# Optimization experiments

Measured on AMD Instinct MI355X. Metric: run time of the kernel, lower is better.

## Reference

```python
import jax, jax.numpy as jnp
import numpy as np

HEAD_SIZE = 8
QK_DIM = 512
V_DIM = 512
N = 4096
ATT_DIM = QK_DIM // HEAD_SIZE  # 64
SCALE = ATT_DIM ** (-0.5)
NEG_FILL = jnp.float32(-9e15)


def setup_inputs() -> dict:
    key = jax.random.key(0)
    k1, k2, k3, k4 = jax.random.split(key, 4)
    x1 = jax.random.normal(k1, (N, QK_DIM), dtype=jnp.float32)
    x2 = jax.random.normal(k2, (N, QK_DIM), dtype=jnp.float32)
    v = jax.random.normal(k3, (N, V_DIM), dtype=jnp.float32)
    adj = jax.random.randint(k4, (N, N), 0, 2, dtype=jnp.int32)
    return {"x1": x1, "x2": x2, "v": v, "adj": adj}


def reference(x1, x2, v, adj):
    n = x1.shape[0]
    # [N, H, d] -> [H, N, d]
    q = x1.reshape(n, HEAD_SIZE, -1).transpose(1, 0, 2) * SCALE
    k = x2.reshape(n, HEAD_SIZE, -1).transpose(1, 0, 2)
    vv = v.reshape(n, HEAD_SIZE, -1).transpose(1, 0, 2)
    # [H, N, N] dense scores, masked by adjacency (broadcast over heads)
    scores = jnp.einsum('hnd,hmd->hnm', q, k)
    scores = jnp.where(adj > 0, scores, NEG_FILL)
    attn = jax.nn.softmax(scores, axis=-1)
    out = jnp.einsum('hnm,hmd->hnd', attn, vv)
    # [H, N, d] -> [N, H*d]
    return out.transpose(1, 0, 2).reshape(n, -1)
```

## Files before the change

kernel.cpp:

```cpp
#include <hip/hip_runtime.h>

#define NN 4096
#define HEADS 8
#define DD 64
#define QKD 512

typedef __attribute__((ext_vector_type(8))) short short8;
typedef __attribute__((ext_vector_type(4))) float f32x4;
typedef __attribute__((ext_vector_type(4))) float float4v;
typedef __attribute__((ext_vector_type(4))) int int4v;
typedef unsigned int u32;
typedef unsigned short u16;
typedef unsigned long long u64;

union U8 { u16 u[8]; short8 s; };
union U4 { u32 u[4]; short8 s; };

__device__ __forceinline__ u16 f2bf(float f) {
  u32 u = __float_as_uint(f);
  u += 0x7fffu + ((u >> 16) & 1u);
  return (u16)(u >> 16);
}

__device__ __forceinline__ u32 cvtpk(float lo, float hi) {
  u32 d;
  asm("v_cvt_pk_bf16_f32 %0, %1, %2" : "=v"(d) : "v"(lo), "v"(hi));
  return d;
}

#define GLL(src, dst) __builtin_amdgcn_global_load_lds( \
    (const __attribute__((address_space(1))) void*)(src), \
    (__attribute__((address_space(3))) void*)(dst), 16, 0, 0)

__global__ __launch_bounds__(256) void prepass_fused(
    const float* __restrict__ x2, const float* __restrict__ v,
    const int* __restrict__ adj,
    u16* __restrict__ Kbt, u16* __restrict__ Vbt, u64* __restrict__ At)
{
  __shared__ u16 Vtmp[64][80];
  const int b = blockIdx.x;
  const int t = threadIdx.x;

  if (b < 4096) {
    const int row = b;
    const int* src = adj + (size_t)row * NN;
    int4v a0 = *(const int4v*)(src + t * 16);
    int4v a1 = *(const int4v*)(src + t * 16 + 4);
    int4v a2 = *(const int4v*)(src + t * 16 + 8);
    int4v a3 = *(const int4v*)(src + t * 16 + 12);
    u32 bits =
        (u32)(a0.x > 0)         | ((u32)(a0.y > 0) << 1)  |
        ((u32)(a0.z > 0) << 2)  | ((u32)(a0.w > 0) << 3)  |
        ((u32)(a1.x > 0) << 4)  | ((u32)(a1.y > 0) << 5)  |
        ((u32)(a1.z > 0) << 6)  | ((u32)(a1.w > 0) << 7)  |
        ((u32)(a2.x > 0) << 8)  | ((u32)(a2.y > 0) << 9)  |
        ((u32)(a2.z > 0) << 10) | ((u32)(a2.w > 0) << 11) |
        ((u32)(a3.x > 0) << 12) | ((u32)(a3.y > 0) << 13) |
        ((u32)(a3.z > 0) << 14) | ((u32)(a3.w > 0) << 15);
    unsigned char* AB = (unsigned char*)Vtmp;
    *(u16*)(AB + t * 2) = (u16)bits;
    __syncthreads();
    if (t < 64) {
      u64 m = *(const u64*)(AB + t * 8);
      At[(size_t)t * NN + row] = m;
    }
  } else if (b < 4608) {
    const int j = b - 4096;
    const int h = j >> 6, kb = j & 63;
    u16* dst = Kbt + (size_t)j * 4096;
    #pragma unroll
    for (int i = 0; i < 2; i++) {
      int c = t + i * 256;
      int off = c * 16;
      int kr = off >> 7;
      int db = (off & 127) ^ ((kr & 7) << 4);
      int d0 = db >> 1;
      const float* p = x2 + (size_t)(kb * 64 + kr) * QKD + h * DD + d0;
      float4v a0 = *(const float4v*)p;
      float4v a1 = *(const float4v*)(p + 4);
      U8 r;
      r.u[0] = f2bf(a0.x); r.u[1] = f2bf(a0.y); r.u[2] = f2bf(a0.z); r.u[3] = f2bf(a0.w);
      r.u[4] = f2bf(a1.x); r.u[5] = f2bf(a1.y); r.u[6] = f2bf(a1.z); r.u[7] = f2bf(a1.w);
      *(short8*)((char*)dst + off) = r.s;
    }
  } else {
    const int bb = b - 4608;
    const int h = bb >> 6, kb = bb & 63;
    {
      int k = t >> 2, j0 = (t & 3) * 16;
      const float* p = v + (size_t)(kb * 64 + k) * QKD + h * DD + j0;
      float4v a0 = *(const float4v*)p;
      float4v a1 = *(const float4v*)(p + 4);
      float4v a2 = *(const float4v*)(p + 8);
      float4v a3 = *(const float4v*)(p + 12);
      U8 r0, r1;
      r0.u[0] = f2bf(a0.x); r0.u[1] = f2bf(a0.y); r0.u[2] = f2bf(a0.z); r0.u[3] = f2bf(a0.w);
      r0.u[4] = f2bf(a1.x); r0.u[5] = f2bf(a1.y); r0.u[6] = f2bf(a1.z); r0.u[7] = f2bf(a1.w);
      r1.u[0] = f2bf(a2.x); r1.u[1] = f2bf(a2.y); r1.u[2] = f2bf(a2.z); r1.u[3] = f2bf(a2.w);
      r1.u[4] = f2bf(a3.x); r1.u[5] = f2bf(a3.y); r1.u[6] = f2bf(a3.z); r1.u[7] = f2bf(a3.w);
      *(short8*)(&Vtmp[k][j0]) = r0.s;
      *(short8*)(&Vtmp[k][j0 + 8]) = r1.s;
    }
    __syncthreads();
    u16* dst = Vbt + (size_t)bb * 4096;
    #pragma unroll
    for (int i = 0; i < 2; i++) {
      int c = t + i * 256;
      int off = c * 16;
      int vd = off >> 7;
      int kbyte = (off & 127) ^ ((vd & 7) << 4);
      int k0 = kbyte >> 1;
      U8 r;
      #pragma unroll
      for (int jj = 0; jj < 8; jj++) r.u[jj] = Vtmp[k0 + jj][vd];
      *(short8*)((char*)dst + off) = r.s;
    }
  }
}

__global__ __launch_bounds__(512, 4) void attn_fast(
    const float* __restrict__ x1,
    const u64* __restrict__ At,
    const u16* __restrict__ Kbt, const u16* __restrict__ Vbt,
    float* __restrict__ out)
{
  __shared__ u16 KL[2][2][4096];
  __shared__ u16 VL[2][2][4096];

  const int b = blockIdx.x;
  const int h = b & 7;
  const int qt = b >> 3;
  const int t = threadIdx.x;
  const int w = t >> 6;
  const int lane = t & 63;
  const int g = lane >> 4;
  const int qi = lane & 15;
  const int qh = w & 3;
  const int kpar = w >> 2;
  const int qrow = qt * 64 + qh * 16 + qi;

  const u16* Ktiles = Kbt + (size_t)h * 64 * 4096;
  const u16* Vtiles = Vbt + (size_t)h * 64 * 4096;

  const float SCL = 0.125f * 1.4426950408889634f;
  short8 qfrag[2];
  #pragma unroll
  for (int dc = 0; dc < 2; dc++) {
    const float* p = x1 + (size_t)qrow * QKD + h * DD + dc * 32 + g * 8;
    float4v a = *(const float4v*)p;
    float4v c = *(const float4v*)(p + 4);
    U8 r;
    r.u[0] = f2bf(a.x * SCL); r.u[1] = f2bf(a.y * SCL);
    r.u[2] = f2bf(a.z * SCL); r.u[3] = f2bf(a.w * SCL);
    r.u[4] = f2bf(c.x * SCL); r.u[5] = f2bf(c.y * SCL);
    r.u[6] = f2bf(c.z * SCL); r.u[7] = f2bf(c.w * SCL);
    qfrag[dc] = r.s;
  }

  const f32x4 zero = {0.f, 0.f, 0.f, 0.f};
  f32x4 Ot[4] = {zero, zero, zero, zero};
  float mrun = -1e30f;
  float lsum = 0.f;

  GLL(Ktiles + 0 * 4096 + t * 8, &KL[0][0][t * 8]);
  GLL(Ktiles + 1 * 4096 + t * 8, &KL[1][0][t * 8]);
  GLL(Vtiles + 0 * 4096 + t * 8, &VL[0][0][t * 8]);
  GLL(Vtiles + 1 * 4096 + t * 8, &VL[1][0][t * 8]);
  u64 adjcur = At[(size_t)kpar * NN + qrow];
  __syncthreads();

  int cur = 0;
  for (int i = 0; i < 32; i++) {
    u64 adjnext = 0;
    if (i < 31) {
      const size_t nt = 2 * (size_t)(i + 1);
      GLL(Ktiles + nt * 4096 + t * 8,       &KL[0][cur ^ 1][t * 8]);
      GLL(Ktiles + (nt + 1) * 4096 + t * 8, &KL[1][cur ^ 1][t * 8]);
      GLL(Vtiles + nt * 4096 + t * 8,       &VL[0][cur ^ 1][t * 8]);
      GLL(Vtiles + (nt + 1) * 4096 + t * 8, &VL[1][cur ^ 1][t * 8]);
      adjnext = At[(nt + kpar) * NN + qrow];
    }

    const char* kbase = (const char*)KL[kpar][cur];
    const char* vbase = (const char*)VL[kpar][cur];
    f32x4 st[4] = {zero, zero, zero, zero};
    __builtin_amdgcn_s_setprio(1);
    #pragma unroll
    for (int tk = 0; tk < 4; tk++) {
      int krow = tk * 16 + qi;
      #pragma unroll
      for (int dc = 0; dc < 2; dc++) {
        int off = (krow * 128 + (dc * 32 + g * 8) * 2) ^ ((krow & 7) << 4);
        short8 af = *(const short8*)(kbase + off);
        st[tk] = __builtin_amdgcn_mfma_f32_16x16x32_bf16(af, qfrag[dc], st[tk], 0, 0, 0);
      }
    }
    __builtin_amdgcn_s_setprio(0);

    u32 blo = (u32)adjcur, bhi = (u32)(adjcur >> 32);

    #pragma unroll
    for (int tk = 0; tk < 4; tk++) {
      u32 half = (tk < 2) ? blo : bhi;
      int bb0 = (tk & 1) * 16 + g * 4;
      #pragma unroll
      for (int r = 0; r < 4; r++) {
        float s = st[tk][r];
        st[tk][r] = ((half >> (bb0 + r)) & 1u) ? s : -9e15f;
      }
    }
    float t0 = fmaxf(fmaxf(st[0][0], st[0][1]), fmaxf(st[0][2], st[0][3]));
    float t1 = fmaxf(fmaxf(st[1][0], st[1][1]), fmaxf(st[1][2], st[1][3]));
    float t2 = fmaxf(fmaxf(st[2][0], st[2][1]), fmaxf(st[2][2], st[2][3]));
    float t3 = fmaxf(fmaxf(st[3][0], st[3][1]), fmaxf(st[3][2], st[3][3]));
    float tmax = fmaxf(fmaxf(t0, t1), fmaxf(t2, t3));
    tmax = fmaxf(tmax, __shfl_xor(tmax, 16));
    tmax = fmaxf(tmax, __shfl_xor(tmax, 32));

    if (!__all(tmax <= mrun)) {
      const float newm = fmaxf(mrun, tmax);
      const float alpha = __builtin_amdgcn_exp2f(mrun - newm);
      lsum *= alpha;
      #pragma unroll
      for (int tv = 0; tv < 4; tv++) {
        Ot[tv][0] *= alpha; Ot[tv][1] *= alpha; Ot[tv][2] *= alpha; Ot[tv][3] *= alpha;
      }
      mrun = newm;
    }

    float psum = 0.f;
    u32 pk[8];
    #pragma unroll
    for (int tk = 0; tk < 4; tk++) {
      float p0 = __builtin_amdgcn_exp2f(st[tk][0] - mrun);
      float p1 = __builtin_amdgcn_exp2f(st[tk][1] - mrun);
      float p2 = __builtin_amdgcn_exp2f(st[tk][2] - mrun);
      float p3 = __builtin_amdgcn_exp2f(st[tk][3] - mrun);
      psum += (p0 + p1) + (p2 + p3);
      pk[tk * 2 + 0] = cvtpk(p0, p1);
      pk[tk * 2 + 1] = cvtpk(p2, p3);
    }
    psum += __shfl_xor(psum, 16);
    psum += __shfl_xor(psum, 32);
    lsum += psum;

    const int srcbase = qi + ((g & 1) << 5);
    #pragma unroll
    for (int kc = 0; kc < 2; kc++) {
      U4 pf;
      #pragma unroll
      for (int jp = 0; jp < 4; jp++) {
        int src = srcbase + ((jp >> 1) << 4);
        u32 va1 = (u32)__shfl((int)pk[4 * kc + (jp & 1)], src);
        u32 vb1 = (u32)__shfl((int)pk[4 * kc + 2 + (jp & 1)], src);
        pf.u[jp] = (g < 2) ? va1 : vb1;
      }
      __builtin_amdgcn_s_setprio(1);
      #pragma unroll
      for (int tv = 0; tv < 4; tv++) {
        int vd = tv * 16 + qi;
        int off = (vd * 128 + (kc * 32 + g * 8) * 2) ^ ((vd & 7) << 4);
        short8 vfrag = *(const short8*)(vbase + off);
        Ot[tv] = __builtin_amdgcn_mfma_f32_16x16x32_bf16(vfrag, pf.s, Ot[tv], 0, 0, 0);
      }
      __builtin_amdgcn_s_setprio(0);
    }

    __syncthreads();
    adjcur = adjnext;
    cur ^= 1;
  }

  float* mb = (float*)&KL[0][0][0];
  const int mbase = (qh * 64 + lane) * 20;
  if (kpar == 1) {
    #pragma unroll
    for (int tv = 0; tv < 4; tv++) {
      mb[mbase + tv * 4 + 0] = Ot[tv][0];
      mb[mbase + tv * 4 + 1] = Ot[tv][1];
      mb[mbase + tv * 4 + 2] = Ot[tv][2];
      mb[mbase + tv * 4 + 3] = Ot[tv][3];
    }
    mb[mbase + 16] = mrun;
    mb[mbase + 17] = lsum;
  }
  __syncthreads();
  if (kpar == 0) {
    const float m2 = mb[mbase + 16];
    const float l2 = mb[mbase + 17];
    const float M = fmaxf(mrun, m2);
    const float a1 = __builtin_amdgcn_exp2f(mrun - M);
    const float a2 = __builtin_amdgcn_exp2f(m2 - M);
    const float inv = 1.0f / (lsum * a1 + l2 * a2);
    #pragma unroll
    for (int tv = 0; tv < 4; tv++) {
      float4v o;
      o.x = (Ot[tv][0] * a1 + mb[mbase + tv * 4 + 0] * a2) * inv;
      o.y = (Ot[tv][1] * a1 + mb[mbase + tv * 4 + 1] * a2) * inv;
      o.z = (Ot[tv][2] * a1 + mb[mbase + tv * 4 + 2] * a2) * inv;
      o.w = (Ot[tv][3] * a1 + mb[mbase + tv * 4 + 3] * a2) * inv;
      *(float4v*)(out + (size_t)qrow * QKD + h * DD + tv * 16 + g * 4) = o;
    }
  }
}

__global__ __launch_bounds__(512) void attn_fallback(
    const float* __restrict__ x1, const float* __restrict__ x2f,
    const float* __restrict__ vf, const int* __restrict__ adj,
    float* __restrict__ out)
{
  __shared__ u16 Klds[64 * 128];
  __shared__ u16 Vlds[128 * 64];
  __shared__ u64 Abits[64];

  const int b = blockIdx.x;
  const int qt = (b & 7) | ((b >> 5) << 3);
  const int hg = (b >> 3) & 3;
  const int h0 = hg * 2;
  const int t = threadIdx.x;
  const int w = t >> 6;
  const int lane = t & 63;
  const int qsub = w >> 1;
  const int hh = w & 1;
  const int h = h0 + hh;
  const int g = lane >> 4;
  const int qi = lane & 15;
  const int qbase = qt * 64;
  const int q_local = qsub * 16 + qi;
  const int qrow = qbase + q_local;

  const float SCL = 0.125f * 1.4426950408889634f;
  short8 qfrag[2];
  #pragma unroll
  for (int dc = 0; dc < 2; dc++) {
    const float* p = x1 + (size_t)qrow * QKD + h * DD + dc * 32 + g * 8;
    float4v a = *(const float4v*)p;
    float4v c = *(const float4v*)(p + 4);
    U8 r;
    r.u[0] = f2bf(a.x * SCL); r.u[1] = f2bf(a.y * SCL);
    r.u[2] = f2bf(a.z * SCL); r.u[3] = f2bf(a.w * SCL);
    r.u[4] = f2bf(c.x * SCL); r.u[5] = f2bf(c.y * SCL);
    r.u[6] = f2bf(c.z * SCL); r.u[7] = f2bf(c.w * SCL);
    qfrag[dc] = r.s;
  }

  const f32x4 zero = {0.f, 0.f, 0.f, 0.f};
  f32x4 Ot[4] = {zero, zero, zero, zero};
  float mrun = -1e30f;
  float lsum = 0.f;

  for (int kb = 0; kb < NN / 64; kb++) {
    const int k0 = kb * 64;
    __syncthreads();
    #pragma unroll
    for (int i = 0; i < 2; i++) {
      int s = t + i * 512;
      int row = s >> 4, c0 = (s & 15) * 8;
      int off = (row * 256 + c0 * 2) ^ ((row & 7) << 4);
      const float* p = x2f + (size_t)(k0 + row) * QKD + h0 * DD + c0;
      float4v a = *(const float4v*)p;
      float4v c = *(const float4v*)(p + 4);
      U8 r;
      r.u[0]=f2bf(a.x); r.u[1]=f2bf(a.y); r.u[2]=f2bf(a.z); r.u[3]=f2bf(a.w);
      r.u[4]=f2bf(c.x); r.u[5]=f2bf(c.y); r.u[6]=f2bf(c.z); r.u[7]=f2bf(c.w);
      *(short8*)((char*)Klds + off) = r.s;
    }
    {
      int vdg = t & 15, kp = t >> 4;
      int vd0 = vdg * 8, kk = kp * 2;
      u16 ua[8], ub[8];
      const float* pa = vf + (size_t)(k0 + kk) * QKD + h0 * DD + vd0;
      float4v a0 = *(const float4v*)pa;
      float4v a1 = *(const float4v*)(pa + 4);
      float4v b0 = *(const float4v*)(pa + QKD);
      float4v b1 = *(const float4v*)(pa + QKD + 4);
      ua[0]=f2bf(a0.x); ua[1]=f2bf(a0.y); ua[2]=f2bf(a0.z); ua[3]=f2bf(a0.w);
      ua[4]=f2bf(a1.x); ua[5]=f2bf(a1.y); ua[6]=f2bf(a1.z); ua[7]=f2bf(a1.w);
      ub[0]=f2bf(b0.x); ub[1]=f2bf(b0.y); ub[2]=f2bf(b0.z); ub[3]=f2bf(b0.w);
      ub[4]=f2bf(b1.x); ub[5]=f2bf(b1.y); ub[6]=f2bf(b1.z); ub[7]=f2bf(b1.w);
      #pragma unroll
      for (int j = 0; j < 8; j++) {
        u32 pk2 = (u32)ua[j] | ((u32)ub[j] << 16);
        int vd = vd0 + j;
        int off = (vd * 128 + kk * 2) ^ (((vd & 7) ^ ((vd >> 3) & 7)) << 4);
        *(u32*)((char*)Vlds + off) = pk2;
      }
    }
    {
      int row = t >> 3, c8 = t & 7;
      const int* ap = adj + (size_t)(qbase + row) * NN + k0 + c8 * 8;
      int4v a0 = *(const int4v*)ap;
      int4v a1 = *(const int4v*)(ap + 4);
      u32 byteval = (u32)(a0.x > 0)        | ((u32)(a0.y > 0) << 1) |
                    ((u32)(a0.z > 0) << 2) | ((u32)(a0.w > 0) << 3) |
                    ((u32)(a1.x > 0) << 4) | ((u32)(a1.y > 0) << 5) |
                    ((u32)(a1.z > 0) << 6) | ((u32)(a1.w > 0) << 7);
      ((unsigned char*)Abits)[row * 8 + c8] = (unsigned char)byteval;
    }
    __syncthreads();

    f32x4 st[4] = {zero, zero, zero, zero};
    #pragma unroll
    for (int tk = 0; tk < 4; tk++) {
      #pragma unroll
      for (int dc = 0; dc < 2; dc++) {
        int krow = tk * 16 + qi;
        int c = hh * 64 + dc * 32 + g * 8;
        int off = (krow * 256 + c * 2) ^ ((krow & 7) << 4);
        short8 af = *(const short8*)((char*)Klds + off);
        st[tk] = __builtin_amdgcn_mfma_f32_16x16x32_bf16(af, qfrag[dc], st[tk], 0, 0, 0);
      }
    }

    u64 bbm = Abits[q_local];
    u32 blo = (u32)bbm, bhi = (u32)(bbm >> 32);

    float tmax = -1e30f;
    #pragma unroll
    for (int tk = 0; tk < 4; tk++) {
      u32 half = (tk < 2) ? blo : bhi;
      int bb0 = (tk & 1) * 16 + g * 4;
      #pragma unroll
      for (int r = 0; r < 4; r++) {
        float s = st[tk][r];
        s = ((half >> (bb0 + r)) & 1u) ? s : -9e15f;
        st[tk][r] = s;
        tmax = fmaxf(tmax, s);
      }
    }
    tmax = fmaxf(tmax, __shfl_xor(tmax, 16));
    tmax = fmaxf(tmax, __shfl_xor(tmax, 32));
    float newm = fmaxf(mrun, tmax);
    float alpha = __builtin_amdgcn_exp2f(mrun - newm);
    mrun = newm;

    float psum = 0.f;
    u32 pk[8];
    #pragma unroll
    for (int tk = 0; tk < 4; tk++) {
      float p0 = __builtin_amdgcn_exp2f(st[tk][0] - newm);
      float p1 = __builtin_amdgcn_exp2f(st[tk][1] - newm);
      float p2 = __builtin_amdgcn_exp2f(st[tk][2] - newm);
      float p3 = __builtin_amdgcn_exp2f(st[tk][3] - newm);
      psum += (p0 + p1) + (p2 + p3);
      pk[tk * 2 + 0] = (u32)f2bf(p0) | ((u32)f2bf(p1) << 16);
      pk[tk * 2 + 1] = (u32)f2bf(p2) | ((u32)f2bf(p3) << 16);
    }
    psum += __shfl_xor(psum, 16);
    psum += __shfl_xor(psum, 32);
    lsum = lsum * alpha + psum;
    #pragma unroll
    for (int tv = 0; tv < 4; tv++) {
      Ot[tv][0] *= alpha; Ot[tv][1] *= alpha; Ot[tv][2] *= alpha; Ot[tv][3] *= alpha;
    }

    const int srcbase = qi + ((g & 1) << 5);
    #pragma unroll
    for (int kc = 0; kc < 2; kc++) {
      U4 pf;
      #pragma unroll
      for (int jp = 0; jp < 4; jp++) {
        int src = srcbase + ((jp >> 1) << 4);
        u32 va1 = (u32)__shfl((int)pk[4 * kc + (jp & 1)], src);
        u32 vb1 = (u32)__shfl((int)pk[4 * kc + 2 + (jp & 1)], src);
        pf.u[jp] = (g < 2) ? va1 : vb1;
      }
      #pragma unroll
      for (int tv = 0; tv < 4; tv++) {
        int vd = hh * 64 + tv * 16 + qi;
        int off = (vd * 128 + (kc * 32 + g * 8) * 2) ^ (((vd & 7) ^ ((vd >> 3) & 7)) << 4);
        short8 vfrag = *(const short8*)((char*)Vlds + off);
        Ot[tv] = __builtin_amdgcn_mfma_f32_16x16x32_bf16(vfrag, pf.s, Ot[tv], 0, 0, 0);
      }
    }
  }

  float inv = 1.0f / lsum;
  #pragma unroll
  for (int tv = 0; tv < 4; tv++) {
    float4v o;
    o.x = Ot[tv][0] * inv; o.y = Ot[tv][1] * inv;
    o.z = Ot[tv][2] * inv; o.w = Ot[tv][3] * inv;
    *(float4v*)(out + (size_t)qrow * QKD + h * DD + tv * 16 + g * 4) = o;
  }
}

extern "C" void kernel_launch(void* const* d_in, const int* in_sizes, int n_in,
                              void* d_out, int out_size, void* d_ws, size_t ws_size,
                              hipStream_t stream) {
  const float* x1 = (const float*)d_in[0];
  const float* x2 = (const float*)d_in[1];
  const float* v  = (const float*)d_in[2];
  const int* adj  = (const int*)d_in[3];
  float* out = (float*)d_out;

  const size_t szK = (size_t)512 * 4096 * sizeof(u16);
  const size_t szV = szK;
  const size_t szA = (size_t)NN * 64 * sizeof(u64);
  const size_t need = szK + szV + szA;

  if (ws_size >= need && d_ws != nullptr) {
    u16* Kbt = (u16*)d_ws;
    u16* Vbt = (u16*)((char*)d_ws + szK);
    u64* At  = (u64*)((char*)d_ws + szK + szV);
    prepass_fused<<<dim3(5120), dim3(256), 0, stream>>>(x2, v, adj, Kbt, Vbt, At);
    attn_fast<<<dim3(512), dim3(512), 0, stream>>>(x1, At, Kbt, Vbt, out);
  } else {
    attn_fallback<<<dim3(256), dim3(512), 0, stream>>>(x1, x2, v, adj, out);
  }
}
```

Measured before the change: 196.2 us.

## Software-pipeline QK^T one tile ahead with triple-buffered K and single-buffered V

The main loop now computes the QK^T MFMAs for tile i+1 before running the mask, softmax and PV of tile i, so matrix work overlaps the exp/shuffle-heavy softmax. K tiles move to a three-slot ring prefetched two tiles ahead, while V is single-buffered: it is loaded at the start of each iteration and guarded by an extra barrier before the PV step. Total LDS stays the same. The trade-off is a second block-wide barrier per iteration, V load latency that is only hidden behind the next-tile QK and softmax, and extra live registers for the carried score tile.

```diff
diff --git a/kernel.cpp b/kernel.cpp
--- a/kernel.cpp
+++ b/kernel.cpp
@@ -124,8 +124,8 @@
     const u16* __restrict__ Kbt, const u16* __restrict__ Vbt,
     float* __restrict__ out)
 {
-  __shared__ u16 KL[2][2][4096];
-  __shared__ u16 VL[2][2][4096];
+  __shared__ u16 KL[2][3][4096];
+  __shared__ u16 VL[2][4096];
 
   const int b = blockIdx.x;
   const int h = b & 7;
@@ -164,26 +164,14 @@
 
   GLL(Ktiles + 0 * 4096 + t * 8, &KL[0][0][t * 8]);
   GLL(Ktiles + 1 * 4096 + t * 8, &KL[1][0][t * 8]);
-  GLL(Vtiles + 0 * 4096 + t * 8, &VL[0][0][t * 8]);
-  GLL(Vtiles + 1 * 4096 + t * 8, &VL[1][0][t * 8]);
-  u64 adjcur = At[(size_t)kpar * NN + qrow];
+  GLL(Ktiles + 2 * 4096 + t * 8, &KL[0][1][t * 8]);
+  GLL(Ktiles + 3 * 4096 + t * 8, &KL[1][1][t * 8]);
+  u64 a_cur = At[(size_t)kpar * NN + qrow];
   __syncthreads();
 
-  int cur = 0;
-  for (int i = 0; i < 32; i++) {
-    u64 adjnext = 0;
-    if (i < 31) {
-      const size_t nt = 2 * (size_t)(i + 1);
-      GLL(Ktiles + nt * 4096 + t * 8,       &KL[0][cur ^ 1][t * 8]);
-      GLL(Ktiles + (nt + 1) * 4096 + t * 8, &KL[1][cur ^ 1][t * 8]);
-      GLL(Vtiles + nt * 4096 + t * 8,       &VL[0][cur ^ 1][t * 8]);
-      GLL(Vtiles + (nt + 1) * 4096 + t * 8, &VL[1][cur ^ 1][t * 8]);
-      adjnext = At[(nt + kpar) * NN + qrow];
-    }
-
-    const char* kbase = (const char*)KL[kpar][cur];
-    const char* vbase = (const char*)VL[kpar][cur];
-    f32x4 st[4] = {zero, zero, zero, zero};
+  f32x4 stC[4] = {zero, zero, zero, zero};
+  {
+    const char* kbase = (const char*)KL[kpar][0];
     __builtin_amdgcn_s_setprio(1);
     #pragma unroll
     for (int tk = 0; tk < 4; tk++) {
@@ -192,12 +180,45 @@
       for (int dc = 0; dc < 2; dc++) {
         int off = (krow * 128 + (dc * 32 + g * 8) * 2) ^ ((krow & 7) << 4);
         short8 af = *(const short8*)(kbase + off);
-        st[tk] = __builtin_amdgcn_mfma_f32_16x16x32_bf16(af, qfrag[dc], st[tk], 0, 0, 0);
+        stC[tk] = __builtin_amdgcn_mfma_f32_16x16x32_bf16(af, qfrag[dc], stC[tk], 0, 0, 0);
       }
     }
     __builtin_amdgcn_s_setprio(0);
-
-    u32 blo = (u32)adjcur, bhi = (u32)(adjcur >> 32);
+  }
+
+  for (int i = 0; i < 32; i++) {
+    if (i < 30) {
+      const int slot = (i + 2) % 3;
+      const size_t kt = 2 * (size_t)(i + 2);
+      GLL(Ktiles + kt * 4096 + t * 8,       &KL[0][slot][t * 8]);
+      GLL(Ktiles + (kt + 1) * 4096 + t * 8, &KL[1][slot][t * 8]);
+    }
+    {
+      const size_t vt = 2 * (size_t)i;
+      GLL(Vtiles + vt * 4096 + t * 8,       &VL[0][t * 8]);
+      GLL(Vtiles + (vt + 1) * 4096 + t * 8, &VL[1][t * 8]);
+    }
+    u64 a_next = 0;
+    if (i < 31) a_next = At[(size_t)(2 * (i + 1) + kpar) * NN + qrow];
+
+    f32x4 stN[4] = {zero, zero, zero, zero};
+    if (i < 31) {
+      const char* kbase = (const char*)KL[kpar][(i + 1) % 3];
+      __builtin_amdgcn_s_setprio(1);
+      #pragma unroll
+      for (int tk = 0; tk < 4; tk++) {
+        int krow = tk * 16 + qi;
+        #pragma unroll
+        for (int dc = 0; dc < 2; dc++) {
+          int off = (krow * 128 + (dc * 32 + g * 8) * 2) ^ ((krow & 7) << 4);
+          short8 af = *(const short8*)(kbase + off);
+          stN[tk] = __builtin_amdgcn_mfma_f32_16x16x32_bf16(af, qfrag[dc], stN[tk], 0, 0, 0);
+        }
+      }
+      __builtin_amdgcn_s_setprio(0);
+    }
+
+    u32 blo = (u32)a_cur, bhi = (u32)(a_cur >> 32);
 
     #pragma unroll
     for (int tk = 0; tk < 4; tk++) {
@@ -205,14 +226,14 @@
       int bb0 = (tk & 1) * 16 + g * 4;
       #pragma unroll
       for (int r = 0; r < 4; r++) {
-        float s = st[tk][r];
-        st[tk][r] = ((half >> (bb0 + r)) & 1u) ? s : -9e15f;
-      }
-    }
-    float t0 = fmaxf(fmaxf(st[0][0], st[0][1]), fmaxf(st[0][2], st[0][3]));
-    float t1 = fmaxf(fmaxf(st[1][0], st[1][1]), fmaxf(st[1][2], st[1][3]));
-    float t2 = fmaxf(fmaxf(st[2][0], st[2][1]), fmaxf(st[2][2], st[2][3]));
-    float t3 = fmaxf(fmaxf(st[3][0], st[3][1]), fmaxf(st[3][2], st[3][3]));
+        float s = stC[tk][r];
+        stC[tk][r] = ((half >> (bb0 + r)) & 1u) ? s : -9e15f;
+      }
+    }
+    float t0 = fmaxf(fmaxf(stC[0][0], stC[0][1]), fmaxf(stC[0][2], stC[0][3]));
+    float t1 = fmaxf(fmaxf(stC[1][0], stC[1][1]), fmaxf(stC[1][2], stC[1][3]));
+    float t2 = fmaxf(fmaxf(stC[2][0], stC[2][1]), fmaxf(stC[2][2], stC[2][3]));
+    float t3 = fmaxf(fmaxf(stC[3][0], stC[3][1]), fmaxf(stC[3][2], stC[3][3]));
     float tmax = fmaxf(fmaxf(t0, t1), fmaxf(t2, t3));
     tmax = fmaxf(tmax, __shfl_xor(tmax, 16));
     tmax = fmaxf(tmax, __shfl_xor(tmax, 32));
@@ -232,10 +253,10 @@
     u32 pk[8];
     #pragma unroll
     for (int tk = 0; tk < 4; tk++) {
-      float p0 = __builtin_amdgcn_exp2f(st[tk][0] - mrun);
-      float p1 = __builtin_amdgcn_exp2f(st[tk][1] - mrun);
-      float p2 = __builtin_amdgcn_exp2f(st[tk][2] - mrun);
-      float p3 = __builtin_amdgcn_exp2f(st[tk][3] - mrun);
+      float p0 = __builtin_amdgcn_exp2f(stC[tk][0] - mrun);
+      float p1 = __builtin_amdgcn_exp2f(stC[tk][1] - mrun);
+      float p2 = __builtin_amdgcn_exp2f(stC[tk][2] - mrun);
+      float p3 = __builtin_amdgcn_exp2f(stC[tk][3] - mrun);
       psum += (p0 + p1) + (p2 + p3);
       pk[tk * 2 + 0] = cvtpk(p0, p1);
       pk[tk * 2 + 1] = cvtpk(p2, p3);
@@ -244,6 +265,9 @@
     psum += __shfl_xor(psum, 32);
     lsum += psum;
 
+    __syncthreads();
+
+    const char* vbase = (const char*)VL[kpar];
     const int srcbase = qi + ((g & 1) << 5);
     #pragma unroll
     for (int kc = 0; kc < 2; kc++) {
@@ -267,8 +291,10 @@
     }
 
     __syncthreads();
-    adjcur = adjnext;
-    cur ^= 1;
+
+    #pragma unroll
+    for (int tk = 0; tk < 4; tk++) stC[tk] = stN[tk];
+    a_cur = a_next;
   }
 
   float* mb = (float*)&KL[0][0][0];
```

Measured after the change: 197.0 us. Within noise of the previous version (+0.4%).
